# Optimization experiments

Measured on AMD Instinct MI355X. Metric: run time of the kernel, lower is better.

## Reference

```python
import jax, jax.numpy as jnp
import numpy as np
import math

N_HEADS = 8
EPS = 1e-12


def _ln(x, g, b):
    m = x.mean(-1, keepdims=True)
    v = ((x - m) ** 2).mean(-1, keepdims=True)
    return (x - m) * jax.lax.rsqrt(v + EPS) * g + b


def _ffn(x, w1, b1, w2, b2):
    # torch nn.GELU default = exact erf gelu; dropout is identity in eval
    return jax.nn.gelu(x @ w1 + b1, approximate=False) @ w2 + b2


def _mha(q_in, kv, mask, qw, qb, kw, kb, vw, vb, ow, ob):
    B, S, _ = q_in.shape
    dh = qw.shape[1] // N_HEADS

    def split(x):
        return x.reshape(B, S, N_HEADS, dh).transpose(0, 2, 1, 3)  # (B,H,S,dh)

    q = split(q_in @ qw + qb) / math.sqrt(dh)
    k = split(kv @ kw + kb)
    v = split(kv @ vw + vb)
    scores = jnp.einsum('bhqd,bhkd->bhqk', q, k) + mask[:, None]
    w = jax.nn.softmax(scores, axis=-1)
    ctx = jnp.einsum('bhqk,bhkd->bhqd', w, v)
    ctx = ctx.transpose(0, 2, 1, 3).reshape(B, S, N_HEADS * dh)
    return ctx @ ow + ob


def reference(hidden, lens,
              f_ffn_w1, f_ffn_b1, f_ffn_w2, f_ffn_b2, f_ln_g, f_ln_b,
              f_q_w, f_q_b, f_k_w, f_k_b, f_v_w, f_v_b, f_o_w, f_o_b,
              b_ffn_w1, b_ffn_b1, b_ffn_w2, b_ffn_b2, b_ln_g, b_ln_b,
              b_q_w, b_q_b, b_k_w, b_k_b, b_v_w, b_v_b, b_o_w, b_o_b,
              attn_ln_g, attn_ln_b,
              out_ffn_w1, out_ffn_b1, out_ffn_w2, out_ffn_b2,
              out_ln_g, out_ln_b):
    S, B, D2 = hidden.shape
    H = D2 // 2
    S2 = S - 2
    f = hidden[..., :H]
    bk = hidden[..., H:]
    query = jnp.concatenate([f[:-2], bk[2:]], axis=-1)        # (S2, B, 2H)
    qbf = jnp.swapaxes(query, 0, 1)                            # (B, S2, 2H)

    # vectorized per-sample length-dependent masks (additive, 0 / -inf)
    qi = jnp.arange(S2)[:, None]
    ki = jnp.arange(S2)[None, :]
    Lm = (lens - 2)[:, None, None]
    # forward: rows >= L-2 all zero; valid rows causal (k <= q) inside [0, L-2)
    f_mask = jnp.where((qi >= Lm) | (ki <= qi), 0.0, -np.inf).astype(hidden.dtype)
    # backward: rows >= L-2 all zero; valid rows anti-causal (k >= q) with k < L-2
    b_mask = jnp.where((qi >= Lm) | ((ki >= qi) & (ki < Lm)), 0.0, -np.inf).astype(hidden.dtype)

    f_q = _ln(_ffn(qbf, f_ffn_w1, f_ffn_b1, f_ffn_w2, f_ffn_b2), f_ln_g, f_ln_b)
    f_kv = jnp.swapaxes(f[:-2], 0, 1)
    f_attn = _mha(f_q, f_kv, f_mask, f_q_w, f_q_b, f_k_w, f_k_b, f_v_w, f_v_b, f_o_w, f_o_b)

    b_q = _ln(_ffn(qbf, b_ffn_w1, b_ffn_b1, b_ffn_w2, b_ffn_b2), b_ln_g, b_ln_b)
    b_kv = jnp.swapaxes(bk[2:], 0, 1)
    b_attn = _mha(b_q, b_kv, b_mask, b_q_w, b_q_b, b_k_w, b_k_b, b_v_w, b_v_b, b_o_w, b_o_b)

    attn_out = _ln(qbf + jnp.concatenate([f_attn, b_attn], axis=-1), attn_ln_g, attn_ln_b)
    out = _ln(_ffn(attn_out, out_ffn_w1, out_ffn_b1, out_ffn_w2, out_ffn_b2), out_ln_g, out_ln_b)
    return jnp.swapaxes(out, 0, 1)                             # (S2, B, 2H)


def setup_inputs():
    key = jax.random.key(0)
    ks = jax.random.split(key, 16)
    S, B, H = 1024, 8, 512
    d = {}
    d['hidden'] = jax.random.normal(ks[0], (S, B, 2 * H), jnp.float32)
    d['lens'] = jax.random.randint(ks[1], (B,), 4, S + 1)

    def w(k, i, o):
        return jax.random.normal(k, (i, o), jnp.float32) * 0.02

    idx = 2
    for p in ('f', 'b'):
        d[p + '_ffn_w1'] = w(ks[idx], 2 * H, 2 * H); idx += 1
        d[p + '_ffn_b1'] = jnp.zeros((2 * H,), jnp.float32)
        d[p + '_ffn_w2'] = w(ks[idx], 2 * H, H); idx += 1
        d[p + '_ffn_b2'] = jnp.zeros((H,), jnp.float32)
        d[p + '_ln_g'] = jnp.ones((H,), jnp.float32)
        d[p + '_ln_b'] = jnp.zeros((H,), jnp.float32)
        for n in ('q', 'k', 'v', 'o'):
            d[p + '_' + n + '_w'] = w(jax.random.fold_in(ks[idx], hash(n) % 97), H, H)
            d[p + '_' + n + '_b'] = jnp.zeros((H,), jnp.float32)
        idx += 1
    d['attn_ln_g'] = jnp.ones((2 * H,), jnp.float32)
    d['attn_ln_b'] = jnp.zeros((2 * H,), jnp.float32)
    d['out_ffn_w1'] = w(ks[idx], 2 * H, 2 * H); idx += 1
    d['out_ffn_b1'] = jnp.zeros((2 * H,), jnp.float32)
    d['out_ffn_w2'] = w(ks[idx], 2 * H, 2 * H); idx += 1
    d['out_ffn_b2'] = jnp.zeros((2 * H,), jnp.float32)
    d['out_ln_g'] = jnp.ones((2 * H,), jnp.float32)
    d['out_ln_b'] = jnp.zeros((2 * H,), jnp.float32)
    return d
```

## Files before the change

kernel.cpp:

```cpp
#include <hip/hip_runtime.h>
#include <cmath>

#define S_ 1024
#define B_ 8
#define H_ 512
#define S2_ 1022
#define M_ (B_*S2_)
#define PAD_ 8192
#define VTS_ ((size_t)8*8*64*1024)

typedef __attribute__((ext_vector_type(8))) short bf16x8;
typedef __attribute__((ext_vector_type(4))) float f32x4;
typedef __attribute__((ext_vector_type(4))) unsigned int u32x4;
typedef __attribute__((ext_vector_type(2))) unsigned int u32x2;

__device__ __forceinline__ unsigned short f2bf(float f){
  unsigned int u = __float_as_uint(f);
  return (unsigned short)((u + 0x7fffu + ((u>>16)&1u)) >> 16);
}
__device__ __forceinline__ float bf2f(unsigned short u){
  return __uint_as_float((unsigned int)u << 16);
}
__device__ __forceinline__ float fgelu(float x){
  float u = x * (0.7978845608f + 0.0356774081f * x * x);
  return x / (1.f + __expf(-2.f * u));
}
__device__ __forceinline__ float fexp2(float x){
  float r; asm("v_exp_f32 %0, %1" : "=v"(r) : "v"(x)); return r;
}
__device__ __forceinline__ unsigned int cvtpk(float lo, float hi){
  unsigned int r; asm("v_cvt_pk_bf16_f32 %0, %1, %2" : "=v"(r) : "v"(lo), "v"(hi)); return r;
}

__device__ __forceinline__ void glds16(const void* g, void* l){
  __builtin_amdgcn_global_load_lds((const __attribute__((address_space(1))) unsigned int*)g,
                                   (__attribute__((address_space(3))) unsigned int*)l, 16, 0, 0);
}
#define SB() __builtin_amdgcn_sched_barrier(0)

__global__ __launch_bounds__(256) void lma_prep_x(const float* __restrict__ hidden,
                                                  unsigned short* __restrict__ Xb){
  int m = blockIdx.x; int dq = threadIdx.x * 4;
  int b = m / S2_, s = m - b * S2_;
  int srow = (dq < 512) ? s : (s + 2);
  const float* src = hidden + ((size_t)srow * B_ + b) * 1024 + dq;
  f32x4 v = *(const f32x4*)src;
  union { u32x2 u; unsigned short s4[4]; } pk;
  #pragma unroll
  for (int j = 0; j < 4; j++) pk.s4[j] = f2bf(v[j]);
  *(u32x2*)&Xb[(size_t)m * 1024 + dq] = pk.u;
}

struct TPack {
  const float* src[14];
  unsigned short* dst[14];
  int K[14];
  int N[14];
};
__global__ __launch_bounds__(256) void lma_transpose_all(TPack p){
  int idx = blockIdx.z;
  int K = p.K[idx], N = p.N[idx];
  int kb = blockIdx.x * 32, nb = blockIdx.y * 32;
  if (kb >= K || nb >= N) return;
  const float* W = p.src[idx];
  unsigned short* WT = p.dst[idx];
  __shared__ float t[32][33];
  int tx = threadIdx.x & 31, ty = threadIdx.x >> 5;
  #pragma unroll
  for (int i = ty; i < 32; i += 8) t[i][tx] = W[(size_t)(kb + i) * N + nb + tx];
  __syncthreads();
  #pragma unroll
  for (int i = ty; i < 32; i += 8) WT[(size_t)(nb + i) * K + kb + tx] = f2bf(t[tx][i]);
}

__global__ __launch_bounds__(256) void lma_biascat(const float* __restrict__ fk, const float* __restrict__ fv,
                                                   const float* __restrict__ bk, const float* __restrict__ bv,
                                                   float* __restrict__ out){
  int i = blockIdx.x * 256 + threadIdx.x;
  int fb = i >> 10, col = i & 1023;
  const float* s = (col < 512) ? (fb ? bk : fk) : (fb ? bv : fv);
  out[i] = s[col & 511];
}

__global__ __launch_bounds__(256) void lma_vt2(const unsigned short* __restrict__ KV2,
                                               unsigned short* __restrict__ VT2){
  __shared__ unsigned short t[32][34];
  int s0 = blockIdx.x * 32, c0 = blockIdx.y * 32;
  int z = blockIdx.z, fb = z >> 3, b = z & 7;
  const unsigned short* V = KV2 + (size_t)fb * PAD_ * 1024 + 512;
  unsigned short* VT = VT2 + (size_t)fb * VTS_;
  int tx = threadIdx.x & 31, ty = threadIdx.x >> 5;
  #pragma unroll
  for (int i = ty; i < 32; i += 8){
    int s = s0 + i; if (s > S2_-1) s = S2_-1;
    t[i][tx] = V[((size_t)b * S2_ + s) * 1024 + c0 + tx];
  }
  __syncthreads();
  int s = s0 + tx;
  #pragma unroll
  for (int i = ty; i < 32; i += 8){
    int c = c0 + i, h = c >> 6, d = c & 63;
    VT[(((size_t)b * 8 + h) * 64 + d) * 1024 + s] = (s < S2_) ? t[tx][i] : (unsigned short)0;
  }
}

__global__ __launch_bounds__(256) void lma_gemm2(
    const unsigned short* __restrict__ A, int lda,
    const unsigned short* __restrict__ Bt0, const unsigned short* __restrict__ Bt1,
    const float* __restrict__ bias0, const float* __restrict__ bias1,
    void* __restrict__ Cout, int ldc,
    int M, int N, int K, int mode, int amap, int nmt)
{
  __shared__ unsigned short Al[128*32];
  __shared__ unsigned short Bl[128*32];
  const int tid = threadIdx.x;
  const int w = tid >> 6, lane = tid & 63, quad = lane >> 4, l16 = lane & 15;
  const int mt = blockIdx.x % nmt, nt = blockIdx.x / nmt;
  const int m0 = mt * 128, n0 = nt * 128;
  const int brch = m0 >> 13;
  const unsigned short* Bt = brch ? Bt1 : Bt0;
  const float* bias = brch ? bias1 : bias0;
  const int coloff = (amap == 2 && brch) ? 512 : 0;
  const int wm = (w >> 1) * 64, wn = (w & 1) * 64;

  f32x4 acc[4][4];
  #pragma unroll
  for (int i = 0; i < 4; i++)
    #pragma unroll
    for (int f = 0; f < 4; f++) acc[i][f] = f32x4{0.f,0.f,0.f,0.f};

  const int srow = lane >> 2;
  const int spc  = (((lane & 3) ^ ((lane >> 2) & 3))) * 8;
  const int rswz = (l16 & 3);

  for (int k0 = 0; k0 < K; k0 += 32) {
    #pragma unroll
    for (int c = 0; c < 2; c++) {
      int ra = w*32 + c*16 + srow;
      int ga = m0 + ra;
      int ar;
      if (amap == 0) { ar = (ga > M-1) ? (M-1) : ga; }
      else { ar = ga & (PAD_-1); if (ar > M_-1) ar = M_-1; }
      glds16(A + (size_t)ar * lda + coloff + k0 + spc, &Al[(w*32 + c*16) * 32]);
      int gb = n0 + ra; if (gb > N-1) gb = N-1;
      glds16(Bt + (size_t)gb * K + k0 + spc, &Bl[(w*32 + c*16) * 32]);
    }
    __syncthreads();
    bf16x8 af[4], bfr[4];
    #pragma unroll
    for (int i = 0; i < 4; i++) af[i]  = *(const bf16x8*)&Al[(wm + i*16 + l16)*32 + ((quad ^ rswz) * 8)];
    #pragma unroll
    for (int f = 0; f < 4; f++) bfr[f] = *(const bf16x8*)&Bl[(wn + f*16 + l16)*32 + ((quad ^ rswz) * 8)];
    #pragma unroll
    for (int i = 0; i < 4; i++)
      #pragma unroll
      for (int f = 0; f < 4; f++)
        acc[i][f] = __builtin_amdgcn_mfma_f32_16x16x32_bf16(af[i], bfr[f], acc[i][f], 0, 0, 0);
    __syncthreads();
  }

  #pragma unroll
  for (int f = 0; f < 4; f++) {
    int col = n0 + wn + f*16 + l16;
    float bv = bias ? bias[col] : 0.f;
    #pragma unroll
    for (int i = 0; i < 4; i++) {
      #pragma unroll
      for (int r = 0; r < 4; r++) {
        int row = m0 + wm + i*16 + quad*4 + r;
        if (row < M) {
          float v = acc[i][f][r] + bv;
          if (mode == 2) v = fgelu(v);
          else if (mode == 1) v *= 0.18033688011112042f;
          if (mode <= 2) ((unsigned short*)Cout)[(size_t)row * ldc + col] = f2bf(v);
          else if (mode == 3) ((float*)Cout)[(size_t)row * ldc + col] = v;
          else {
            int sr = row % S2_, bb2 = row / S2_;
            ((float*)Cout)[((size_t)sr * B_ + bb2) * ldc + col] = v;
          }
        }
      }
    }
  }
}

__global__ __launch_bounds__(512, 2) void lma_gemm8(
    const unsigned short* __restrict__ A, int lda,
    const unsigned short* __restrict__ Bt0, const unsigned short* __restrict__ Bt1,
    const float* __restrict__ bias0, const float* __restrict__ bias1,
    unsigned short* __restrict__ Cout, int ldc,
    int M, int N, int K, int mode, int amap, int nmt)
{
  __shared__ unsigned short Ls[2][2][256*64];
  const int tid = threadIdx.x;
  const int w = tid >> 6, lane = tid & 63, quad = lane >> 4, l16 = lane & 15;
  const int mt = blockIdx.x % nmt, nt = blockIdx.x / nmt;
  const int m0 = mt * 256, n0 = nt * 256;
  const int brch = m0 >> 13;
  const unsigned short* Bt = brch ? Bt1 : Bt0;
  const float* bias = brch ? bias1 : bias0;
  const int coloff = (amap == 2 && brch) ? 512 : 0;
  const int wm = (w >> 2) * 128, wn = (w & 3) * 64;

  f32x4 acc[8][4];
  #pragma unroll
  for (int i = 0; i < 8; i++)
    #pragma unroll
    for (int f = 0; f < 4; f++) acc[i][f] = f32x4{0.f,0.f,0.f,0.f};

  const int lrow8 = lane >> 3;
  const int lkb   = lane & 7;
  const int NT = K >> 6;

  const unsigned short* aP[2][2]; const unsigned short* bP[2][2];
  int aD[2][2], bD[2][2];
  #pragma unroll
  for (int hf = 0; hf < 2; hf++)
    #pragma unroll
    for (int c = 0; c < 2; c++) {
      int rtA = (w>>2)*128 + hf*64 + ((w&3)*2 + c)*8 + lrow8;
      int kbA = lkb ^ (((rtA>>2)&3)<<1);
      int ga = m0 + rtA;
      int ar;
      if (amap == 0) { ar = (ga > M-1) ? (M-1) : ga; }
      else { ar = ga & (PAD_-1); if (ar > M_-1) ar = M_-1; }
      aP[hf][c] = A + (size_t)ar * lda + coloff + kbA*8;
      aD[hf][c] = ((w>>2)*128 + hf*64 + ((w&3)*2 + c)*8) * 64;
      int rtB = (w>>1)*64 + hf*32 + ((w&1)*2 + c)*8 + lrow8;
      int kbB = lkb ^ (((rtB>>2)&3)<<1);
      int gb = n0 + rtB; if (gb > N-1) gb = N-1;
      bP[hf][c] = Bt + (size_t)gb * K + kbB*8;
      bD[hf][c] = ((w>>1)*64 + hf*32 + ((w&1)*2 + c)*8) * 64;
    }

  bf16x8 af[4][2], bf[2][2];

  #define STA(buf, hf, kt) { _Pragma("unroll") for (int c = 0; c < 2; c++) \
      glds16(aP[hf][c] + (size_t)(kt)*64, &Ls[buf][0][aD[hf][c]]); }
  #define STB(buf, hf, kt) { _Pragma("unroll") for (int c = 0; c < 2; c++) \
      glds16(bP[hf][c] + (size_t)(kt)*64, &Ls[buf][1][bD[hf][c]]); }
  #define LDA8(buf, mq) { _Pragma("unroll") for (int j = 0; j < 4; j++){ \
      int rt = wm + (mq)*64 + j*16 + l16; \
      const unsigned short* base = &Ls[buf][0][rt*64]; \
      int f_ = ((rt>>2)&3)<<1; \
      af[j][0] = *(const bf16x8*)(base + ((    quad) ^ f_)*8); \
      af[j][1] = *(const bf16x8*)(base + ((4 + quad) ^ f_)*8); } }
  #define LDB8(buf, nq) { _Pragma("unroll") for (int j = 0; j < 2; j++){ \
      int rt = wn + (nq)*32 + j*16 + l16; \
      const unsigned short* base = &Ls[buf][1][rt*64]; \
      int f_ = ((rt>>2)&3)<<1; \
      bf[j][0] = *(const bf16x8*)(base + ((    quad) ^ f_)*8); \
      bf[j][1] = *(const bf16x8*)(base + ((4 + quad) ^ f_)*8); } }
  #define MFMAQ(mq, nq) { __builtin_amdgcn_s_setprio(1); \
      _Pragma("unroll") for (int j = 0; j < 4; j++) \
        _Pragma("unroll") for (int j2 = 0; j2 < 2; j2++){ \
          acc[(mq)*4+j][(nq)*2+j2] = __builtin_amdgcn_mfma_f32_16x16x32_bf16(af[j][0], bf[j2][0], acc[(mq)*4+j][(nq)*2+j2], 0, 0, 0); \
          acc[(mq)*4+j][(nq)*2+j2] = __builtin_amdgcn_mfma_f32_16x16x32_bf16(af[j][1], bf[j2][1], acc[(mq)*4+j][(nq)*2+j2], 0, 0, 0); } \
      __builtin_amdgcn_s_setprio(0); }
  #define BAR()   { SB(); __builtin_amdgcn_s_barrier(); SB(); }
  #define LGKM0() { asm volatile("s_waitcnt lgkmcnt(0)" ::: "memory"); SB(); }
  #define VM6()   { asm volatile("s_waitcnt vmcnt(6)"   ::: "memory"); SB(); }
  #define VM2()   { asm volatile("s_waitcnt vmcnt(2)"   ::: "memory"); SB(); }

  STA(0, 0, 0); STB(0, 0, 0); STB(0, 1, 0); STA(0, 1, 0);
  STA(1, 0, 1);
  asm volatile("s_waitcnt vmcnt(2)" ::: "memory"); SB();
  BAR();

  const int NI = NT >> 1;
  for (int i = 0; i < NI; i++) {
    const int tb  = 2*i + 1;
    int ta2 = 2*i + 2; if (ta2 > NT-1) ta2 = NT-1;
    int tb2 = 2*i + 3; if (tb2 > NT-1) tb2 = NT-1;

    LDA8(0, 0); LDB8(0, 0); STB(1, 0, tb); STB(1, 1, tb); STA(1, 1, tb);
    BAR(); LGKM0(); MFMAQ(0, 0); BAR();
    LDB8(0, 1); STA(0, 0, ta2);
    BAR(); LGKM0(); MFMAQ(0, 1); BAR();
    LDA8(0, 1); STB(0, 1, ta2);
    BAR(); LGKM0(); MFMAQ(1, 1); BAR();
    LDB8(0, 0); STA(0, 1, ta2);
    BAR(); LGKM0(); MFMAQ(1, 0); VM6(); BAR();
    LDA8(1, 0); LDB8(1, 0); STB(0, 0, ta2);
    BAR(); LGKM0(); MFMAQ(0, 0); BAR();
    LDB8(1, 1); STA(1, 0, tb2);
    BAR(); LGKM0(); MFMAQ(0, 1); BAR();
    LDA8(1, 1);
    BAR(); LGKM0(); MFMAQ(1, 1); BAR();
    LDB8(1, 0);
    BAR(); LGKM0(); MFMAQ(1, 0); VM2(); BAR();
  }
  asm volatile("s_waitcnt vmcnt(0)" ::: "memory");

  #pragma unroll
  for (int f = 0; f < 4; f++) {
    int col = n0 + wn + f*16 + l16;
    float bv = bias ? bias[col] : 0.f;
    #pragma unroll
    for (int i2 = 0; i2 < 8; i2++) {
      #pragma unroll
      for (int r = 0; r < 4; r++) {
        int row = m0 + wm + i2*16 + quad*4 + r;
        if (row < M) {
          float v = acc[i2][f][r] + bv;
          if (mode == 2) v = fgelu(v);
          Cout[(size_t)row * ldc + col] = f2bf(v);
        }
      }
    }
  }
  #undef STA
  #undef STB
  #undef LDA8
  #undef LDB8
  #undef MFMAQ
  #undef BAR
  #undef LGKM0
  #undef VM6
  #undef VM2
}

__device__ __forceinline__ void lma_red2(float& s, float& sq){
  __shared__ float red[16];
  #pragma unroll
  for (int msk = 1; msk < 64; msk <<= 1){ s += __shfl_xor(s, msk); sq += __shfl_xor(sq, msk); }
  int w = threadIdx.x >> 6;
  if ((threadIdx.x & 63) == 0){ red[w] = s; red[8 + w] = sq; }
  __syncthreads();
  s  = red[0] + red[1] + red[2] + red[3];
  sq = red[8] + red[9] + red[10] + red[11];
}

__global__ __launch_bounds__(256) void lma_ln(const float* __restrict__ in,
                                              const float* __restrict__ g, const float* __restrict__ bb,
                                              int D, unsigned short* __restrict__ obf, float* __restrict__ of32){
  int row = blockIdx.x, t = threadIdx.x;
  const float* x = in + (size_t)row * D;
  float s = 0.f, sq = 0.f;
  for (int d = t; d < D; d += 256){ float v = x[d]; s += v; sq += v * v; }
  lma_red2(s, sq);
  float mean = s / D;
  float var = sq / D - mean * mean;
  float rstd = rsqrtf(fmaxf(var, 0.f) + 1e-12f);
  if (obf) {
    for (int d = t; d < D; d += 256) obf[(size_t)row * D + d] = f2bf((x[d] - mean) * rstd * g[d] + bb[d]);
  } else {
    for (int d = t; d < D; d += 256) of32[(size_t)row * D + d] = (x[d] - mean) * rstd * g[d] + bb[d];
  }
}

__global__ __launch_bounds__(256) void lma_ln2(const unsigned short* __restrict__ T12b,
                                               const float* __restrict__ fg, const float* __restrict__ fbb,
                                               const float* __restrict__ bg, const float* __restrict__ bbb,
                                               unsigned short* __restrict__ LQ2){
  int m = blockIdx.x, t = threadIdx.x;
  int fb = (m >= M_);
  int idx = m - fb * M_;
  const float* g = fb ? bg : fg;
  const float* bb = fb ? bbb : fbb;
  const unsigned short* x = T12b + ((size_t)fb * PAD_ + idx) * 512;
  unsigned short* o = LQ2 + ((size_t)fb * PAD_ + idx) * 512;
  float v0 = bf2f(x[t]), v1 = bf2f(x[t + 256]);
  float s = v0 + v1, sq = v0*v0 + v1*v1;
  lma_red2(s, sq);
  float mean = s / 512.f;
  float var = sq / 512.f - mean * mean;
  float rstd = rsqrtf(fmaxf(var, 0.f) + 1e-12f);
  o[t]       = f2bf((v0 - mean) * rstd * g[t]       + bb[t]);
  o[t + 256] = f2bf((v1 - mean) * rstd * g[t + 256] + bb[t + 256]);
}

__global__ __launch_bounds__(256) void lma_attn_ln(const unsigned short* __restrict__ pf,
                                                   const unsigned short* __restrict__ pb,
                                                   const float* __restrict__ hidden,
                                                   const float* __restrict__ g, const float* __restrict__ bb,
                                                   unsigned short* __restrict__ out){
  int m = blockIdx.x, t = threadIdx.x;
  int b = m / S2_, s = m - b * S2_;
  const float* hf = hidden + ((size_t)s       * B_ + b) * 1024;
  const float* hb = hidden + ((size_t)(s + 2) * B_ + b) * 1024;
  float v[4]; float sum = 0.f, sq = 0.f;
  #pragma unroll
  for (int j = 0; j < 4; j++){
    int d = t + j * 256;
    float x = (d < 512) ? (bf2f(pf[(size_t)m * 512 + d]) + hf[d])
                        : (bf2f(pb[(size_t)m * 512 + (d - 512)]) + hb[d]);
    v[j] = x; sum += x; sq += x * x;
  }
  lma_red2(sum, sq);
  float mean = sum / 1024.f;
  float var = sq / 1024.f - mean * mean;
  float rstd = rsqrtf(fmaxf(var, 0.f) + 1e-12f);
  #pragma unroll
  for (int j = 0; j < 4; j++){
    int d = t + j * 256;
    out[(size_t)m * 1024 + d] = f2bf((v[j] - mean) * rstd * g[d] + bb[d]);
  }
}

__global__ __launch_bounds__(256, 4) void lma_attn9(const unsigned short* __restrict__ Q2,
                                                    const unsigned short* __restrict__ KV2,
                                                    const unsigned short* __restrict__ VT2,
                                                    unsigned short* __restrict__ CT2,
                                                    const int* __restrict__ lens,
                                                    int fb){
  __shared__ unsigned short Kl[64*64];
  __shared__ unsigned short Vl[64*64];
  __shared__ __align__(16) unsigned short Pl[4][16*64];

  const int tid = threadIdx.x;
  const int w = tid >> 6, lane = tid & 63, quad = lane >> 4, l16 = lane & 15;
  const int id = blockIdx.x;
  const int qi = id >> 6;
  const int qt = (int)((0x8ACE75319BDF6420ull >> (qi*4)) & 15ull);
  const int h = (id >> 3) & 7, b = id & 7;
  const int backward = fb;
  const int L2 = lens[b] - 2;
  const int q0wg = qt * 64;
  const int q0 = q0wg + w * 16;
  const int qg = q0 + l16;
  const int qload = (qg > S2_-1) ? (S2_-1) : qg;

  const size_t qbase  = ((size_t)b * S2_) * 512  + h * 64;
  const size_t kbase  = ((size_t)b * S2_) * 1024 + h * 64;
  const size_t vtbase = ((size_t)(b * 8 + h) * 64) * 1024;
  char* Pb = (char*)&Pl[w][0];

  const int lrow = lane >> 3;
  const int g0s  = (lane & 7) ^ lrow;
  const int x7   = l16 & 7;
  const int x7s  = x7 << 4;

  const unsigned short* Q  = Q2  + (size_t)fb * PAD_ * 512;
  const unsigned short* Kx = KV2 + (size_t)fb * PAD_ * 1024;
  const unsigned short* VT = VT2 + (size_t)fb * VTS_;
  unsigned short* CTX      = CT2 + (size_t)fb * PAD_ * 512;

  bf16x8 qf[2];
  {
    const unsigned short* qp = Q + qbase + (size_t)qload * 512 + quad * 8;
    qf[0] = *(const bf16x8*)(qp);
    qf[1] = *(const bf16x8*)(qp + 32);
  }

  float mi = -3e38f, li = 0.f;
  f32x4 ot[4];
  #pragma unroll
  for (int f = 0; f < 4; f++) ot[f] = f32x4{0.f,0.f,0.f,0.f};

  int klo = 0, khi = S2_ - 1;
  if (q0wg + 63 < L2) {
    if (!backward) khi = q0wg + 63;
    else { klo = q0wg; khi = L2 - 1; }
  }

  for (int kt0 = klo; kt0 <= khi; kt0 += 64) {
    #pragma unroll
    for (int c = 0; c < 2; c++) {
      int r = w*16 + c*8 + lrow;
      int kr = kt0 + r; if (kr > S2_-1) kr = S2_-1;
      glds16(Kx + kbase + (size_t)kr * 1024 + g0s * 8, &Kl[(w*16 + c*8) * 64]);
      glds16(VT + vtbase + (size_t)r * 1024 + kt0 + g0s * 8, &Vl[(w*16 + c*8) * 64]);
    }
    __syncthreads();

    bf16x8 kf[4][2], vf[4][2];
    #pragma unroll
    for (int sub = 0; sub < 4; sub++) {
      const unsigned short* kp = &Kl[(sub*16 + l16) * 64];
      kf[sub][0] = *(const bf16x8*)(kp + (( quad      ^ x7) * 8));
      kf[sub][1] = *(const bf16x8*)(kp + (((quad + 4) ^ x7) * 8));
    }
    #pragma unroll
    for (int f = 0; f < 4; f++) {
      const unsigned short* vp = &Vl[(f*16 + l16) * 64];
      vf[f][0] = *(const bf16x8*)(vp + (( quad      ^ x7) * 8));
      vf[f][1] = *(const bf16x8*)(vp + (((quad + 4) ^ x7) * 8));
    }

    f32x4 st[4];
    __builtin_amdgcn_s_setprio(1);
    #pragma unroll
    for (int sub = 0; sub < 4; sub++) {
      f32x4 s = f32x4{0.f,0.f,0.f,0.f};
      s = __builtin_amdgcn_mfma_f32_16x16x32_bf16(kf[sub][0], qf[0], s, 0, 0, 0);
      s = __builtin_amdgcn_mfma_f32_16x16x32_bf16(kf[sub][1], qf[1], s, 0, 0, 0);
      st[sub] = s;
    }
    __builtin_amdgcn_s_setprio(0);

    {
      bool tail = (kt0 + 63 > S2_ - 1);
      bool full;
      if (!backward) full = !tail && ((kt0 + 63 <= q0) || (q0 >= L2));
      else           full = !tail && ((q0 >= L2) || ((kt0 >= q0 + 15) && (kt0 + 63 < L2)));
      if (!full) {
        #pragma unroll
        for (int sub = 0; sub < 4; sub++) {
          #pragma unroll
          for (int r = 0; r < 4; r++) {
            int kg = kt0 + sub*16 + quad*4 + r;
            bool ok;
            if (!backward) ok = (kg < S2_) && ((qg >= L2) || (kg <= qg));
            else           ok = (kg < S2_) && ((qg >= L2) || ((kg >= qg) && (kg < L2)));
            if (!ok) st[sub][r] = -3e38f;
          }
        }
      }
    }

    float mx = -3e38f;
    #pragma unroll
    for (int sub = 0; sub < 4; sub++)
      #pragma unroll
      for (int r = 0; r < 4; r++) mx = fmaxf(mx, st[sub][r]);
    mx = fmaxf(mx, __shfl_xor(mx, 16));
    mx = fmaxf(mx, __shfl_xor(mx, 32));

    if (__any(mx > mi + 11.f)) {
      float mn = fmaxf(mi, mx);
      float al = fexp2(mi - mn);
      li *= al;
      #pragma unroll
      for (int f = 0; f < 4; f++)
        #pragma unroll
        for (int r = 0; r < 4; r++) ot[f][r] *= al;
      mi = mn;
    }

    float rs = 0.f;
    #pragma unroll
    for (int sub = 0; sub < 4; sub++)
      #pragma unroll
      for (int r = 0; r < 4; r++) {
        float p = fexp2(st[sub][r] - mi);
        st[sub][r] = p; rs += p;
      }
    rs += __shfl_xor(rs, 16);
    rs += __shfl_xor(rs, 32);
    li += rs;

    #pragma unroll
    for (int sub = 0; sub < 4; sub++) {
      u32x2 pk2;
      pk2[0] = cvtpk(st[sub][0], st[sub][1]);
      pk2[1] = cvtpk(st[sub][2], st[sub][3]);
      *(u32x2*)(Pb + (l16*128 + ((sub*32 + quad*8) ^ x7s))) = pk2;
    }
    bf16x8 pfr0 = *(const bf16x8*)(Pb + (l16*128 + (( 0 + quad*16) ^ x7s)));
    bf16x8 pfr1 = *(const bf16x8*)(Pb + (l16*128 + ((64 + quad*16) ^ x7s)));

    __builtin_amdgcn_s_setprio(1);
    #pragma unroll
    for (int f = 0; f < 4; f++) {
      ot[f] = __builtin_amdgcn_mfma_f32_16x16x32_bf16(vf[f][0], pfr0, ot[f], 0, 0, 0);
      ot[f] = __builtin_amdgcn_mfma_f32_16x16x32_bf16(vf[f][1], pfr1, ot[f], 0, 0, 0);
    }
    __builtin_amdgcn_s_setprio(0);
    __syncthreads();
  }

  if (qg < S2_) {
    float rcp = 1.f / li;
    #pragma unroll
    for (int f = 0; f < 4; f++) {
      ushort4 pk;
      pk.x = f2bf(ot[f][0] * rcp); pk.y = f2bf(ot[f][1] * rcp);
      pk.z = f2bf(ot[f][2] * rcp); pk.w = f2bf(ot[f][3] * rcp);
      *(ushort4*)&CTX[qbase + (size_t)qg * 512 + f*16 + quad*4] = pk;
    }
  }
}

extern "C" void kernel_launch(void* const* d_in, const int* in_sizes, int n_in,
                              void* d_out, int out_size, void* d_ws, size_t ws_size,
                              hipStream_t stream)
{
  const float* hidden = (const float*)d_in[0];
  const int*   lens   = (const int*)d_in[1];
  const float* fw[14]; for (int i = 0; i < 14; i++) fw[i] = (const float*)d_in[2 + i];
  const float* bw[14]; for (int i = 0; i < 14; i++) bw[i] = (const float*)d_in[16 + i];
  const float* attn_g = (const float*)d_in[30];
  const float* attn_b = (const float*)d_in[31];
  const float* o_w1 = (const float*)d_in[32];
  const float* o_b1 = (const float*)d_in[33];
  const float* o_w2 = (const float*)d_in[34];
  const float* o_b2 = (const float*)d_in[35];
  const float* o_lng = (const float*)d_in[36];
  const float* o_lnb = (const float*)d_in[37];

  char* ws = (char*)d_ws;
  size_t off = 0;
  auto alloc = [&](size_t bytes)->char* {
    off = (off + 255) & ~(size_t)255;
    char* p = ws + off; off += bytes; return p;
  };

  unsigned short* fw1t = (unsigned short*)alloc((size_t)1024*1024*2);
  unsigned short* fw2t = (unsigned short*)alloc((size_t)512*1024*2);
  unsigned short* fqt  = (unsigned short*)alloc((size_t)512*512*2);
  unsigned short* fkvt = (unsigned short*)alloc((size_t)1024*512*2);
  unsigned short* fot  = (unsigned short*)alloc((size_t)512*512*2);
  unsigned short* bw1t = (unsigned short*)alloc((size_t)1024*1024*2);
  unsigned short* bw2t = (unsigned short*)alloc((size_t)512*1024*2);
  unsigned short* bqt  = (unsigned short*)alloc((size_t)512*512*2);
  unsigned short* bkvt = (unsigned short*)alloc((size_t)1024*512*2);
  unsigned short* bot  = (unsigned short*)alloc((size_t)512*512*2);
  unsigned short* ow1t = (unsigned short*)alloc((size_t)1024*1024*2);
  unsigned short* ow2t = (unsigned short*)alloc((size_t)1024*1024*2);
  float*          biasKV = (float*)alloc(2048*4);

  unsigned short* Xb   = (unsigned short*)alloc((size_t)M_*1024*2);
  unsigned short* big1 = (unsigned short*)alloc((size_t)2*PAD_*1024*2);
  float*          big2 = (float*)alloc((size_t)2*PAD_*512*4);
  unsigned short* LQCT = (unsigned short*)alloc((size_t)2*PAD_*512*2);
  unsigned short* Q2   = (unsigned short*)alloc((size_t)2*PAD_*512*2);

  unsigned short* H12 = big1, *KV2 = big1, *H1o = big1;
  unsigned short* T12b = (unsigned short*)big2;
  unsigned short* VT2  = (unsigned short*)big2;
  unsigned short* P2b  = (unsigned short*)big2 + 2*VTS_;
  unsigned short* LQ2 = LQCT, *CT2 = LQCT;

  lma_prep_x<<<M_, 256, 0, stream>>>(hidden, Xb);

  {
    TPack tp;
    const float* srcs[14] = { fw[0], fw[2], fw[6], fw[8], fw[10], fw[12],
                              bw[0], bw[2], bw[6], bw[8], bw[10], bw[12],
                              o_w1, o_w2 };
    unsigned short* dsts[14] = { fw1t, fw2t, fqt, fkvt, fkvt + (size_t)512*512, fot,
                                 bw1t, bw2t, bqt, bkvt, bkvt + (size_t)512*512, bot,
                                 ow1t, ow2t };
    int Ks[14] = {1024,1024,512,512,512,512, 1024,1024,512,512,512,512, 1024,1024};
    int Ns[14] = {1024, 512,512,512,512,512, 1024, 512,512,512,512,512, 1024,1024};
    for (int i = 0; i < 14; i++){ tp.src[i]=srcs[i]; tp.dst[i]=dsts[i]; tp.K[i]=Ks[i]; tp.N[i]=Ns[i]; }
    lma_transpose_all<<<dim3(32, 32, 14), 256, 0, stream>>>(tp);
  }
  lma_biascat<<<8, 256, 0, stream>>>(fw[9], fw[11], bw[9], bw[11], biasKV);

  auto G = [&](const unsigned short* A, int lda,
               const unsigned short* B0, const unsigned short* B1,
               const float* b0, const float* b1,
               void* C, int ldc, int M, int N, int K, int mode, int amap){
    int nmt = (M + 127) / 128;
    lma_gemm2<<<dim3(nmt * (N/128)), 256, 0, stream>>>(A, lda, B0, B1, b0, b1, C, ldc, M, N, K, mode, amap, nmt);
  };
  auto G8 = [&](const unsigned short* A, int lda,
                const unsigned short* B0, const unsigned short* B1,
                const float* b0, const float* b1,
                unsigned short* C, int ldc, int M, int N, int K, int mode, int amap){
    int nmt = M / 256;
    lma_gemm8<<<dim3(nmt * (N/256)), 512, 0, stream>>>(A, lda, B0, B1, b0, b1, C, ldc, M, N, K, mode, amap, nmt);
  };

  G8(Xb, 1024, fw1t, bw1t, fw[1], bw[1], H12, 1024, 2*PAD_, 1024, 1024, 2, 1);
  G(H12, 1024, fw2t, bw2t, fw[3], bw[3], T12b, 512, 2*PAD_, 512, 1024, 0, 0);
  lma_ln2<<<2*M_, 256, 0, stream>>>(T12b, fw[4], fw[5], bw[4], bw[5], LQ2);
  G(LQ2, 512, fqt, bqt, fw[7], bw[7], Q2, 512, 2*PAD_, 512, 512, 1, 0);
  G8(Xb, 1024, fkvt, bkvt, biasKV, biasKV + 1024, KV2, 1024, 2*PAD_, 1024, 512, 0, 2);
  lma_vt2<<<dim3(32, 16, 16), 256, 0, stream>>>(KV2, VT2);

  lma_attn9<<<dim3(1024), 256, 0, stream>>>(Q2, KV2, VT2, CT2, lens, 0);
  lma_attn9<<<dim3(1024), 256, 0, stream>>>(Q2, KV2, VT2, CT2, lens, 1);

  G(CT2, 512, fot, bot, fw[13], bw[13], P2b, 512, 2*PAD_, 512, 512, 0, 0);

  lma_attn_ln<<<M_, 256, 0, stream>>>(P2b, P2b + (size_t)PAD_*512, hidden, attn_g, attn_b, Xb);

  G(Xb, 1024, ow1t, ow1t, o_b1, o_b1, H1o, 1024, M_, 1024, 1024, 2, 0);
  G(H1o, 1024, ow2t, ow2t, o_b2, o_b2, (float*)d_out, 1024, M_, 1024, 1024, 4, 0);
  lma_ln<<<M_, 256, 0, stream>>>((float*)d_out, o_lng, o_lnb, 1024, nullptr, (float*)d_out);
}
```

Before: 638.0 us.

## Retune LDS swizzles, reorder GEMM load schedule, reorder epilogue, linearize attention tiles

Changes the LDS XOR swizzle patterns in both GEMM kernels to reduce bank conflicts on fragment reads. It also spreads the global-to-LDS loads in the 256-tile GEMM more evenly across the MFMA phases and adds extra vmcnt waits. The epilogue loop order is swapped so each row's four column fragments are written together. The attention kernel drops its permuted query-tile ordering in favour of plain linear order, which may alter load balancing across the causal masks.

```diff
diff --git a/kernel.cpp b/kernel.cpp
--- a/kernel.cpp
+++ b/kernel.cpp
@@ -130,8 +130,8 @@
     for (int f = 0; f < 4; f++) acc[i][f] = f32x4{0.f,0.f,0.f,0.f};
 
   const int srow = lane >> 2;
-  const int spc  = (((lane & 3) ^ ((lane >> 2) & 3))) * 8;
-  const int rswz = (l16 & 3);
+  const int spc  = (((lane & 3) ^ ((lane >> 3) & 3))) * 8;
+  const int rswz = (l16 >> 1) & 3;
 
   for (int k0 = 0; k0 < K; k0 += 32) {
     #pragma unroll
@@ -159,24 +159,26 @@
     __syncthreads();
   }
 
-  #pragma unroll
-  for (int f = 0; f < 4; f++) {
-    int col = n0 + wn + f*16 + l16;
-    float bv = bias ? bias[col] : 0.f;
-    #pragma unroll
-    for (int i = 0; i < 4; i++) {
-      #pragma unroll
-      for (int r = 0; r < 4; r++) {
-        int row = m0 + wm + i*16 + quad*4 + r;
-        if (row < M) {
-          float v = acc[i][f][r] + bv;
+  float bv[4];
+  #pragma unroll
+  for (int f = 0; f < 4; f++) bv[f] = bias ? bias[n0 + wn + f*16 + l16] : 0.f;
+  const int col0 = n0 + wn + l16;
+  #pragma unroll
+  for (int i = 0; i < 4; i++) {
+    #pragma unroll
+    for (int r = 0; r < 4; r++) {
+      int row = m0 + wm + i*16 + quad*4 + r;
+      if (row < M) {
+        #pragma unroll
+        for (int f = 0; f < 4; f++) {
+          float v = acc[i][f][r] + bv[f];
           if (mode == 2) v = fgelu(v);
           else if (mode == 1) v *= 0.18033688011112042f;
-          if (mode <= 2) ((unsigned short*)Cout)[(size_t)row * ldc + col] = f2bf(v);
-          else if (mode == 3) ((float*)Cout)[(size_t)row * ldc + col] = v;
+          if (mode <= 2) ((unsigned short*)Cout)[(size_t)row * ldc + col0 + f*16] = f2bf(v);
+          else if (mode == 3) ((float*)Cout)[(size_t)row * ldc + col0 + f*16] = v;
           else {
             int sr = row % S2_, bb2 = row / S2_;
-            ((float*)Cout)[((size_t)sr * B_ + bb2) * ldc + col] = v;
+            ((float*)Cout)[((size_t)sr * B_ + bb2) * ldc + col0 + f*16] = v;
           }
         }
       }
@@ -219,7 +221,7 @@
     #pragma unroll
     for (int c = 0; c < 2; c++) {
       int rtA = (w>>2)*128 + hf*64 + ((w&3)*2 + c)*8 + lrow8;
-      int kbA = lkb ^ (((rtA>>2)&3)<<1);
+      int kbA = lkb ^ (rtA & 7);
       int ga = m0 + rtA;
       int ar;
       if (amap == 0) { ar = (ga > M-1) ? (M-1) : ga; }
@@ -227,7 +229,7 @@
       aP[hf][c] = A + (size_t)ar * lda + coloff + kbA*8;
       aD[hf][c] = ((w>>2)*128 + hf*64 + ((w&3)*2 + c)*8) * 64;
       int rtB = (w>>1)*64 + hf*32 + ((w&1)*2 + c)*8 + lrow8;
-      int kbB = lkb ^ (((rtB>>2)&3)<<1);
+      int kbB = lkb ^ (rtB & 7);
       int gb = n0 + rtB; if (gb > N-1) gb = N-1;
       bP[hf][c] = Bt + (size_t)gb * K + kbB*8;
       bD[hf][c] = ((w>>1)*64 + hf*32 + ((w&1)*2 + c)*8) * 64;
@@ -242,13 +244,13 @@
   #define LDA8(buf, mq) { _Pragma("unroll") for (int j = 0; j < 4; j++){ \
       int rt = wm + (mq)*64 + j*16 + l16; \
       const unsigned short* base = &Ls[buf][0][rt*64]; \
-      int f_ = ((rt>>2)&3)<<1; \
+      int f_ = rt & 7; \
       af[j][0] = *(const bf16x8*)(base + ((    quad) ^ f_)*8); \
       af[j][1] = *(const bf16x8*)(base + ((4 + quad) ^ f_)*8); } }
   #define LDB8(buf, nq) { _Pragma("unroll") for (int j = 0; j < 2; j++){ \
       int rt = wn + (nq)*32 + j*16 + l16; \
       const unsigned short* base = &Ls[buf][1][rt*64]; \
-      int f_ = ((rt>>2)&3)<<1; \
+      int f_ = rt & 7; \
       bf[j][0] = *(const bf16x8*)(base + ((    quad) ^ f_)*8); \
       bf[j][1] = *(const bf16x8*)(base + ((4 + quad) ^ f_)*8); } }
   #define MFMAQ(mq, nq) { __builtin_amdgcn_s_setprio(1); \
@@ -273,38 +275,40 @@
     int ta2 = 2*i + 2; if (ta2 > NT-1) ta2 = NT-1;
     int tb2 = 2*i + 3; if (tb2 > NT-1) tb2 = NT-1;
 
-    LDA8(0, 0); LDB8(0, 0); STB(1, 0, tb); STB(1, 1, tb); STA(1, 1, tb);
+    LDA8(0, 0); LDB8(0, 0); STB(1, 0, tb);
     BAR(); LGKM0(); MFMAQ(0, 0); BAR();
-    LDB8(0, 1); STA(0, 0, ta2);
+    LDB8(0, 1); STB(1, 1, tb);
     BAR(); LGKM0(); MFMAQ(0, 1); BAR();
-    LDA8(0, 1); STB(0, 1, ta2);
+    LDA8(0, 1); STA(1, 1, tb);
     BAR(); LGKM0(); MFMAQ(1, 1); BAR();
-    LDB8(0, 0); STA(0, 1, ta2);
+    LDB8(0, 0); STA(0, 0, ta2);
     BAR(); LGKM0(); MFMAQ(1, 0); VM6(); BAR();
-    LDA8(1, 0); LDB8(1, 0); STB(0, 0, ta2);
-    BAR(); LGKM0(); MFMAQ(0, 0); BAR();
-    LDB8(1, 1); STA(1, 0, tb2);
-    BAR(); LGKM0(); MFMAQ(0, 1); BAR();
-    LDA8(1, 1);
+    LDA8(1, 0); LDB8(1, 0); STB(0, 1, ta2);
+    BAR(); LGKM0(); MFMAQ(0, 0); VM6(); BAR();
+    LDB8(1, 1); STA(0, 1, ta2);
+    BAR(); LGKM0(); MFMAQ(0, 1); VM6(); BAR();
+    LDA8(1, 1); STB(0, 0, ta2);
     BAR(); LGKM0(); MFMAQ(1, 1); BAR();
-    LDB8(1, 0);
+    LDB8(1, 0); STA(1, 0, tb2);
     BAR(); LGKM0(); MFMAQ(1, 0); VM2(); BAR();
   }
   asm volatile("s_waitcnt vmcnt(0)" ::: "memory");
 
-  #pragma unroll
-  for (int f = 0; f < 4; f++) {
-    int col = n0 + wn + f*16 + l16;
-    float bv = bias ? bias[col] : 0.f;
-    #pragma unroll
-    for (int i2 = 0; i2 < 8; i2++) {
-      #pragma unroll
-      for (int r = 0; r < 4; r++) {
-        int row = m0 + wm + i2*16 + quad*4 + r;
-        if (row < M) {
-          float v = acc[i2][f][r] + bv;
+  float bv[4];
+  #pragma unroll
+  for (int f = 0; f < 4; f++) bv[f] = bias ? bias[n0 + wn + f*16 + l16] : 0.f;
+  const int col0 = n0 + wn + l16;
+  #pragma unroll
+  for (int i2 = 0; i2 < 8; i2++) {
+    #pragma unroll
+    for (int r = 0; r < 4; r++) {
+      int row = m0 + wm + i2*16 + quad*4 + r;
+      if (row < M) {
+        #pragma unroll
+        for (int f = 0; f < 4; f++) {
+          float v = acc[i2][f][r] + bv[f];
           if (mode == 2) v = fgelu(v);
-          Cout[(size_t)row * ldc + col] = f2bf(v);
+          Cout[(size_t)row * ldc + col0 + f*16] = f2bf(v);
         }
       }
     }
@@ -411,9 +415,7 @@
   const int tid = threadIdx.x;
   const int w = tid >> 6, lane = tid & 63, quad = lane >> 4, l16 = lane & 15;
   const int id = blockIdx.x;
-  const int qi = id >> 6;
-  const int qt = (int)((0x8ACE75319BDF6420ull >> (qi*4)) & 15ull);
-  const int h = (id >> 3) & 7, b = id & 7;
+  const int qt = id >> 6, h = (id >> 3) & 7, b = id & 7;
   const int backward = fb;
   const int L2 = lens[b] - 2;
   const int q0wg = qt * 64;
```

Result: faster. 568.9 us (-10.8%).
